# Optimization experiments

Hardware: AMD Instinct MI355X
Metric: run time of the kernel (lower is better)

The kernel has to match this reference:

```python
import jax, jax.numpy as jnp
import numpy as np
from jax import lax

TAU = 0.1
EPS = 1e-10


def setup_inputs() -> dict:
    key = jax.random.key(0)
    ks = jax.random.split(key, 9)
    T, B, I, H, O = 512, 128, 512, 512, 512
    std = 1.0 / np.sqrt(H)
    x = jax.random.normal(ks[0], (T, B, I), dtype=jnp.float32)
    # uniform noise for per-step gumbel-softmax sampling (training mode)
    gumbel_u = jax.random.uniform(ks[1], (T, H, 2), dtype=jnp.float32,
                                  minval=1e-6, maxval=1.0 - 1e-6)
    # parameters (orthogonal init approximated by scaled normal)
    W_in = jax.random.normal(ks[2], (H, I), dtype=jnp.float32) * std
    b_in = jax.random.normal(ks[3], (H,), dtype=jnp.float32) * std
    Wrec_free = jax.nn.relu(jax.random.normal(ks[4], (H, H), dtype=jnp.float32) * std)
    rec_bias = jax.random.normal(ks[5], (H,), dtype=jnp.float32) * std
    eimask_logit = jax.random.normal(ks[6], (H, 2), dtype=jnp.float32)
    W_out = jax.random.normal(ks[7], (O, H), dtype=jnp.float32) * std
    b_out = jax.random.normal(ks[8], (O,), dtype=jnp.float32) * std
    return {"x": x, "gumbel_u": gumbel_u, "W_in": W_in, "b_in": b_in,
            "Wrec_free": Wrec_free, "rec_bias": rec_bias,
            "eimask_logit": eimask_logit, "W_out": W_out, "b_out": b_out}


def reference(x, gumbel_u, W_in, b_in, Wrec_free, rec_bias, eimask_logit, W_out, b_out):
    # x: (T, B, I); gumbel_u: (T, H, 2)
    B = x.shape[1]
    H = W_in.shape[0]
    # gumbel-softmax (soft, tau=0.1) per timestep -> ei code in [-1, 1]
    g = -jnp.log(-jnp.log(gumbel_u + EPS) + EPS)                 # (T, H, 2)
    mask = jax.nn.softmax((eimask_logit[None] + g) / TAU, axis=-1)
    ei = mask[..., 0] - mask[..., 1]                              # (T, H)
    Wrec = jax.nn.relu(Wrec_free)                                 # (H, H)
    # precompute input gate for all steps: (T, B, H)
    ig = jnp.einsum('tbi,hi->tbh', x, W_in) + b_in

    def step(h, inp):
        ig_t, ei_t = inp
        # h @ (Wrec @ diag(ei)).T == (h * ei) @ Wrec.T
        rec_in = (h * ei_t) @ Wrec.T + rec_bias
        h_new = jax.nn.softplus(ig_t + rec_in)
        return h_new, h_new

    h0 = jnp.zeros((B, H), dtype=x.dtype)
    h_last, hs = lax.scan(step, h0, (ig, ei))                     # hs: (T, B, H)
    outputs = jnp.einsum('tbh,oh->tbo', hs, W_out) + b_out        # (T, B, O)
    c_last = jnp.zeros_like(h_last)                               # c is never updated
    return outputs, h_last, c_last
```

## Files before the change

kernel.cpp:

```cpp
#include <hip/hip_runtime.h>
#include <stdint.h>


typedef __attribute__((ext_vector_type(8))) short short8;
typedef __attribute__((ext_vector_type(4))) float f32x4;
typedef __attribute__((ext_vector_type(4))) int int4x;

#if __has_builtin(__builtin_amdgcn_sdot4)
#define SDOT4(a, b, c) __builtin_amdgcn_sdot4((a), (b), (c), false)
#else
__device__ __forceinline__ int sdot4_asm(int a, int b, int c) {
  int r;
  asm volatile("v_dot4_i32_i8 %0, %1, %2, %3"
               : "=v"(r) : "v"(a), "v"(b), "v"(c));
  return r;
}
#define SDOT4(a, b, c) sdot4_asm((a), (b), (c))
#endif

__device__ __forceinline__ unsigned short f2b(float f) {
  unsigned int u = __float_as_uint(f);
  u = (u + 0x7fffu + ((u >> 16) & 1u)) >> 16;
  return (unsigned short)u;
}
__device__ __forceinline__ float b2f(unsigned short s) {
  return __uint_as_float(((unsigned int)s) << 16);
}

__global__ void prep_kernel(const float* __restrict__ gu,
                            const float* __restrict__ logit,
                            const float* __restrict__ win,
                            const float* __restrict__ wout,
                            float* __restrict__ ei,
                            unsigned short* __restrict__ winb,
                            unsigned short* __restrict__ woutb,
                            float* __restrict__ c_last) {
  int i = blockIdx.x * 256 + threadIdx.x;
  int h = i & 511;
  float u0 = gu[2 * i], u1 = gu[2 * i + 1];
  float l0 = logit[2 * h], l1 = logit[2 * h + 1];
  float g0 = -logf(-logf(u0 + 1e-10f) + 1e-10f);
  float g1 = -logf(-logf(u1 + 1e-10f) + 1e-10f);
  float dz = ((l0 + g0) - (l1 + g1)) * 10.0f;
  ei[i] = tanhf(0.5f * dz);
  winb[i]  = f2b(win[i]);
  woutb[i] = f2b(wout[i]);
  if (i < 65536) c_last[i] = 0.0f;
}

__global__ void wquant_kernel(const float* __restrict__ wrec,
                              char* __restrict__ wrec8,
                              float* __restrict__ wscale) {
  const int n = blockIdx.x;
  const int l = threadIdx.x;
  const float* row = wrec + (size_t)n * 512 + l * 8;
  float v[8];
  float m = 0.f;
#pragma unroll
  for (int e = 0; e < 8; ++e) {
    v[e] = fmaxf(row[e], 0.f);
    m = fmaxf(m, v[e]);
  }
#pragma unroll
  for (int off = 32; off >= 1; off >>= 1) m = fmaxf(m, __shfl_down(m, off));
  m = __shfl(m, 0);
  const float s = (m > 0.f) ? (m / 127.f) : 1.f;
  const float inv = 1.f / s;
  unsigned long long pk = 0;
#pragma unroll
  for (int e = 0; e < 8; ++e) {
    int q = (int)rintf(v[e] * inv);
    pk |= ((unsigned long long)(unsigned char)(char)q) << (8 * e);
  }
  *(unsigned long long*)(wrec8 + (size_t)n * 512 + l * 8) = pk;
  if (l == 0) wscale[n] = s;
}

template <int A_F32, int OUT_BF16>
__global__ __launch_bounds__(256, 2) void gemm512(
    const void* __restrict__ Ap, const unsigned short* __restrict__ W,
    const float* __restrict__ bias, void* __restrict__ Cp) {
  __shared__ __align__(16) unsigned short Al[128][32];
  __shared__ __align__(16) unsigned short Bl[128][32];
  const int tid = threadIdx.x;
  const int w = tid >> 6, l = tid & 63;
  const int wr = w >> 1, wc = w & 1;
  const int lm = l & 15, lq = l >> 4;
  const size_t m0 = (size_t)blockIdx.x * 128;
  const int n0 = blockIdx.y * 128;
  const int r = tid >> 1;
  const int sb = (tid & 1) << 1;
  f32x4 acc[4][4] = {};

  for (int kt = 0; kt < 16; ++kt) {
    const int k0 = kt << 5;
    {
      char* dst = (char*)Al + r * 64;
      if (A_F32) {
        const float* A = (const float*)Ap + (m0 + r) * 512 + k0 + (sb << 3);
#pragma unroll
        for (int j = 0; j < 2; ++j) {
          float4 v0 = ((const float4*)A)[2 * j + 0];
          float4 v1 = ((const float4*)A)[2 * j + 1];
          short8 o;
          o[0] = (short)f2b(v0.x); o[1] = (short)f2b(v0.y);
          o[2] = (short)f2b(v0.z); o[3] = (short)f2b(v0.w);
          o[4] = (short)f2b(v1.x); o[5] = (short)f2b(v1.y);
          o[6] = (short)f2b(v1.z); o[7] = (short)f2b(v1.w);
          *(short8*)(dst + (((sb + j + (r >> 1)) & 3) << 4)) = o;
        }
      } else {
        const unsigned short* A =
            (const unsigned short*)Ap + (m0 + r) * 512 + k0 + (sb << 3);
#pragma unroll
        for (int j = 0; j < 2; ++j)
          *(short8*)(dst + (((sb + j + (r >> 1)) & 3) << 4)) =
              *(const short8*)(A + 8 * j);
      }
      const unsigned short* Wp = W + ((size_t)(n0 + r) << 9) + k0 + (sb << 3);
      char* dstB = (char*)Bl + r * 64;
#pragma unroll
      for (int j = 0; j < 2; ++j)
        *(short8*)(dstB + (((sb + j + (r >> 1)) & 3) << 4)) =
            *(const short8*)(Wp + 8 * j);
    }
    __syncthreads();
    short8 af[4], bf[4];
#pragma unroll
    for (int i = 0; i < 4; ++i) {
      int row = wr * 64 + i * 16 + lm;
      af[i] = *(const short8*)((char*)Al + row * 64 +
                               (((lq + (row >> 1)) & 3) << 4));
    }
#pragma unroll
    for (int j = 0; j < 4; ++j) {
      int row = wc * 64 + j * 16 + lm;
      bf[j] = *(const short8*)((char*)Bl + row * 64 +
                               (((lq + (row >> 1)) & 3) << 4));
    }
#pragma unroll
    for (int i = 0; i < 4; ++i)
#pragma unroll
      for (int j = 0; j < 4; ++j)
        acc[i][j] =
            __builtin_amdgcn_mfma_f32_16x16x32_bf16(af[i], bf[j], acc[i][j], 0, 0, 0);
    __syncthreads();
  }
  float bv[4];
#pragma unroll
  for (int j = 0; j < 4; ++j) bv[j] = bias[n0 + wc * 64 + j * 16 + lm];
#pragma unroll
  for (int i = 0; i < 4; ++i) {
#pragma unroll
    for (int r4 = 0; r4 < 4; ++r4) {
      size_t gm = m0 + wr * 64 + i * 16 + lq * 4 + r4;
#pragma unroll
      for (int j = 0; j < 4; ++j) {
        int gn = n0 + wc * 64 + j * 16 + lm;
        float v = acc[i][j][r4] + bv[j];
        if (OUT_BF16)
          ((unsigned short*)Cp)[(gm << 9) + gn] = f2b(v);
        else
          ((float*)Cp)[(gm << 9) + gn] = v;
      }
    }
  }
}

__global__ __launch_bounds__(512, 2) void recur11_kernel(
    const unsigned short* __restrict__ ig,
    const float* __restrict__ ei,
    const char* __restrict__ wrec8,
    const float* __restrict__ wscale,
    const float* __restrict__ rbias,
    unsigned short* __restrict__ hs,
    float* __restrict__ h_last) {
  __shared__ __align__(16) char As[2][512];
  const int tid = threadIdx.x;
  const int g = blockIdx.x;
  const int n = tid;

  int4x wregs[32];
#pragma unroll
  for (int d = 0; d < 32; ++d)
    wregs[d] = *(const int4x*)(wrec8 + ((size_t)n << 9) + (d << 4));
  const float wscv = wscale[n] * 0.0625f;
  const float rbv  = rbias[n];
  if (tid < 256) ((int*)As)[tid] = 0;
  __syncthreads();

  const unsigned short* igp = ig + ((size_t)g << 9) + n;
  unsigned short ig_cur = igp[0];
  float ei_cur = ei[512 + n];

#pragma unroll 1
  for (int t = 0; t < 512; ++t) {
    const int par = t & 1, par2 = par ^ 1;
    unsigned short ig_nxt = 0;
    float ei_nxt = 0.f;
    if (t < 511)
      ig_nxt = __builtin_nontemporal_load(igp + (size_t)(t + 1) * 65536);
    if (t < 510) ei_nxt = ei[(size_t)(t + 2) * 512 + n];

    const char* ap = &As[par][0];
    int ac0 = 0, ac1 = 0, ac2 = 0, ac3 = 0;
#pragma unroll
    for (int d = 0; d < 32; ++d) {
      int4x a4 = *(const int4x*)(ap + (d << 4));
      ac0 = SDOT4(a4[0], wregs[d][0], ac0);
      ac1 = SDOT4(a4[1], wregs[d][1], ac1);
      ac2 = SDOT4(a4[2], wregs[d][2], ac2);
      ac3 = SDOT4(a4[3], wregs[d][3], ac3);
    }
    const int acci = (ac0 + ac1) + (ac2 + ac3);

    float z = (float)acci * wscv + b2f(ig_cur) + rbv;
    float az = fabsf(z);
    float h = fmaxf(z, 0.f) + __logf(1.f + __expf(-az));
    if (t < 511) {
      float a = h * ei_cur * 16.f;
      int ai = (int)rintf(fminf(fmaxf(a, -127.f), 127.f));
      As[par2][n] = (char)ai;
    }
    __builtin_nontemporal_store(f2b(h),
                                hs + (((size_t)t * 128 + g) << 9) + n);
    if (t == 511) h_last[((size_t)g << 9) + n] = h;
    ig_cur = ig_nxt;
    ei_cur = ei_nxt;
    __syncthreads();
  }
}

extern "C" void kernel_launch(void* const* d_in, const int* in_sizes, int n_in,
                              void* d_out, int out_size, void* d_ws,
                              size_t ws_size, hipStream_t stream) {
  const float* x     = (const float*)d_in[0];
  const float* gu    = (const float*)d_in[1];
  const float* Win   = (const float*)d_in[2];
  const float* bin   = (const float*)d_in[3];
  const float* Wrec  = (const float*)d_in[4];
  const float* rbias = (const float*)d_in[5];
  const float* elog  = (const float*)d_in[6];
  const float* Wout  = (const float*)d_in[7];
  const float* bout  = (const float*)d_in[8];

  char* ws = (char*)d_ws;
  float* ei             = (float*)ws;
  unsigned short* winb  = (unsigned short*)(ws + 4194304);
  unsigned short* woutb = (unsigned short*)(ws + 4718592);
  char* wrec8           = (char*)(ws + 5242880);
  float* wscale         = (float*)(ws + 5505024);
  unsigned short* igb   = (unsigned short*)(ws + 6291456);
  unsigned short* hs    = (unsigned short*)(ws + 73400320);

  float* outp  = (float*)d_out;
  float* hlast = outp + 33554432;
  float* clast = outp + 33554432 + 65536;

  prep_kernel<<<1024, 256, 0, stream>>>(gu, elog, Win, Wout, ei, winb, woutb,
                                        clast);
  wquant_kernel<<<512, 64, 0, stream>>>(Wrec, wrec8, wscale);
  gemm512<1, 1><<<dim3(512, 4), 256, 0, stream>>>(x, winb, bin, igb);
  recur11_kernel<<<128, 512, 0, stream>>>(igb, ei, wrec8, wscale, rbias, hs,
                                          hlast);
  gemm512<0, 0><<<dim3(512, 4), 256, 0, stream>>>(hs, woutb, bout, outp);
}
```

Baseline: 600.0 us.

## Broadcast recurrent activations via scalar loads from global instead of LDS

Each step's int8 activation vector now lives in a per-block global buffer rather than LDS. It is read with s_load_dwordx16 into scalar registers after invalidating the scalar cache, so every lane's dot4 uses SGPR operands. The aim is to remove per-thread LDS vector reads and VGPR pressure from the sequential inner loop, with the loads split into staged batches. The trade-off is that each step now depends on an L2 round trip through the scalar cache. It also relies on the barrier to make the vector stores visible to scalar loads.

```diff
diff --git a/kernel.cpp b/kernel.cpp
--- a/kernel.cpp
+++ b/kernel.cpp
@@ -5,6 +5,7 @@
 typedef __attribute__((ext_vector_type(8))) short short8;
 typedef __attribute__((ext_vector_type(4))) float f32x4;
 typedef __attribute__((ext_vector_type(4))) int int4x;
+typedef __attribute__((ext_vector_type(16))) int i32x16;
 
 #if __has_builtin(__builtin_amdgcn_sdot4)
 #define SDOT4(a, b, c) __builtin_amdgcn_sdot4((a), (b), (c), false)
@@ -17,6 +18,32 @@
 }
 #define SDOT4(a, b, c) sdot4_asm((a), (b), (c))
 #endif
+
+#define SLOAD16(dst, base, OFF) \
+  asm volatile("s_load_dwordx16 %0, %1, " #OFF : "=s"(dst) : "s"(base))
+#define SWAIT2(va, vb)                                          \
+  do {                                                          \
+    asm volatile("s_waitcnt lgkmcnt(0)" : "+s"(va), "+s"(vb));  \
+    __builtin_amdgcn_sched_barrier(0);                          \
+  } while (0)
+#define DOT16(sv, wb) do {                       \
+    ac0 = SDOT4(sv[0],  wregs[(wb)+0][0], ac0);  \
+    ac1 = SDOT4(sv[1],  wregs[(wb)+0][1], ac1);  \
+    ac2 = SDOT4(sv[2],  wregs[(wb)+0][2], ac2);  \
+    ac3 = SDOT4(sv[3],  wregs[(wb)+0][3], ac3);  \
+    ac0 = SDOT4(sv[4],  wregs[(wb)+1][0], ac0);  \
+    ac1 = SDOT4(sv[5],  wregs[(wb)+1][1], ac1);  \
+    ac2 = SDOT4(sv[6],  wregs[(wb)+1][2], ac2);  \
+    ac3 = SDOT4(sv[7],  wregs[(wb)+1][3], ac3);  \
+    ac0 = SDOT4(sv[8],  wregs[(wb)+2][0], ac0);  \
+    ac1 = SDOT4(sv[9],  wregs[(wb)+2][1], ac1);  \
+    ac2 = SDOT4(sv[10], wregs[(wb)+2][2], ac2);  \
+    ac3 = SDOT4(sv[11], wregs[(wb)+2][3], ac3);  \
+    ac0 = SDOT4(sv[12], wregs[(wb)+3][0], ac0);  \
+    ac1 = SDOT4(sv[13], wregs[(wb)+3][1], ac1);  \
+    ac2 = SDOT4(sv[14], wregs[(wb)+3][2], ac2);  \
+    ac3 = SDOT4(sv[15], wregs[(wb)+3][3], ac3);  \
+  } while (0)
 
 __device__ __forceinline__ unsigned short f2b(float f) {
   unsigned int u = __float_as_uint(f);
@@ -167,15 +194,15 @@
   }
 }
 
-__global__ __launch_bounds__(512, 2) void recur11_kernel(
+__global__ __launch_bounds__(512, 1) void recur12_kernel(
     const unsigned short* __restrict__ ig,
     const float* __restrict__ ei,
     const char* __restrict__ wrec8,
     const float* __restrict__ wscale,
     const float* __restrict__ rbias,
     unsigned short* __restrict__ hs,
+    char* __restrict__ aglob,
     float* __restrict__ h_last) {
-  __shared__ __align__(16) char As[2][512];
   const int tid = threadIdx.x;
   const int g = blockIdx.x;
   const int n = tid;
@@ -186,7 +213,9 @@
     wregs[d] = *(const int4x*)(wrec8 + ((size_t)n << 9) + (d << 4));
   const float wscv = wscale[n] * 0.0625f;
   const float rbv  = rbias[n];
-  if (tid < 256) ((int*)As)[tid] = 0;
+
+  char* abase = aglob + ((size_t)g << 10);
+  if (tid < 256) ((int*)abase)[tid] = 0;
   __syncthreads();
 
   const unsigned short* igp = ig + ((size_t)g << 9) + n;
@@ -202,16 +231,26 @@
       ig_nxt = __builtin_nontemporal_load(igp + (size_t)(t + 1) * 65536);
     if (t < 510) ei_nxt = ei[(size_t)(t + 2) * 512 + n];
 
-    const char* ap = &As[par][0];
+    asm volatile("s_dcache_inv" ::: "memory");
+    const void* ap = abase + (par << 9);
+    i32x16 c0a, c0b, c1a, c1b, c2a, c2b, c3a, c3b;
     int ac0 = 0, ac1 = 0, ac2 = 0, ac3 = 0;
-#pragma unroll
-    for (int d = 0; d < 32; ++d) {
-      int4x a4 = *(const int4x*)(ap + (d << 4));
-      ac0 = SDOT4(a4[0], wregs[d][0], ac0);
-      ac1 = SDOT4(a4[1], wregs[d][1], ac1);
-      ac2 = SDOT4(a4[2], wregs[d][2], ac2);
-      ac3 = SDOT4(a4[3], wregs[d][3], ac3);
-    }
+    SLOAD16(c0a, ap, 0);
+    SLOAD16(c0b, ap, 64);
+    SLOAD16(c1a, ap, 128);
+    SLOAD16(c1b, ap, 192);
+    SWAIT2(c0a, c0b);
+    DOT16(c0a, 0); DOT16(c0b, 4);
+    SWAIT2(c1a, c1b);
+    SLOAD16(c2a, ap, 256);
+    SLOAD16(c2b, ap, 320);
+    DOT16(c1a, 8); DOT16(c1b, 12);
+    SWAIT2(c2a, c2b);
+    SLOAD16(c3a, ap, 384);
+    SLOAD16(c3b, ap, 448);
+    DOT16(c2a, 16); DOT16(c2b, 20);
+    SWAIT2(c3a, c3b);
+    DOT16(c3a, 24); DOT16(c3b, 28);
     const int acci = (ac0 + ac1) + (ac2 + ac3);
 
     float z = (float)acci * wscv + b2f(ig_cur) + rbv;
@@ -220,7 +259,7 @@
     if (t < 511) {
       float a = h * ei_cur * 16.f;
       int ai = (int)rintf(fminf(fmaxf(a, -127.f), 127.f));
-      As[par2][n] = (char)ai;
+      abase[(par2 << 9) + n] = (char)ai;
     }
     __builtin_nontemporal_store(f2b(h),
                                 hs + (((size_t)t * 128 + g) << 9) + n);
@@ -250,6 +289,7 @@
   unsigned short* woutb = (unsigned short*)(ws + 4718592);
   char* wrec8           = (char*)(ws + 5242880);
   float* wscale         = (float*)(ws + 5505024);
+  char* aglob           = (char*)(ws + 5509120);
   unsigned short* igb   = (unsigned short*)(ws + 6291456);
   unsigned short* hs    = (unsigned short*)(ws + 73400320);
 
@@ -261,7 +301,7 @@
                                         clast);
   wquant_kernel<<<512, 64, 0, stream>>>(Wrec, wrec8, wscale);
   gemm512<1, 1><<<dim3(512, 4), 256, 0, stream>>>(x, winb, bin, igb);
-  recur11_kernel<<<128, 512, 0, stream>>>(igb, ei, wrec8, wscale, rbias, hs,
-                                          hlast);
+  recur12_kernel<<<128, 512, 0, stream>>>(igb, ei, wrec8, wscale, rbias, hs,
+                                          aglob, hlast);
   gemm512<0, 0><<<dim3(512, 4), 256, 0, stream>>>(hs, woutb, bout, outp);
 }
```

Result: slower. 699.5 us (+16.6%).
